# Optimization experiments

Hardware: AMD Instinct MI355X
Metric: run time of the kernel (lower is better)

The kernel has to match this reference:

```python
import jax, jax.numpy as jnp
import numpy as np
import math

B, S, D, H = 4, 2048, 1024, 16
HD = D // H

def setup_inputs() -> dict:
    key = jax.random.key(0)
    k = jax.random.split(key, 5)
    scale = 1.0 / math.sqrt(D)
    return {
        "x": jax.random.normal(k[0], (B, S, D), dtype=jnp.float32),
        "W_qkv": jax.random.normal(k[1], (D, 3 * D), dtype=jnp.float32) * scale,
        "b_qkv": jnp.zeros((3 * D,), dtype=jnp.float32),
        "W_out": jax.random.normal(k[2], (D, D), dtype=jnp.float32) * scale,
        "b_out": jnp.zeros((D,), dtype=jnp.float32),
    }

def reference(x, W_qkv, b_qkv, W_out, b_out):
    b, s, d = x.shape
    qkv = x @ W_qkv + b_qkv                       # [b, s, 3d]
    qkv = qkv.reshape(b, s, 3, H, HD)
    q, k, v = jnp.moveaxis(qkv, 2, 0)             # each [b, s, H, HD]
    q = jnp.transpose(q, (0, 2, 1, 3))            # [b, H, s, hd]
    k = jnp.transpose(k, (0, 2, 1, 3))
    v = jnp.transpose(v, (0, 2, 1, 3))
    scores = jnp.einsum('bhqd,bhkd->bhqk', q, k) / math.sqrt(HD)
    causal = jnp.tril(jnp.ones((s, s), dtype=bool))
    scores = jnp.where(causal, scores, -jnp.inf)
    weights = jax.nn.softmax(scores, axis=-1)     # dropout = identity (eval)
    attended = jnp.einsum('bhqk,bhkd->bhqd', weights, v)
    attended = jnp.transpose(attended, (0, 2, 1, 3)).reshape(b, s, d)
    return attended @ W_out + b_out
```

## Files before the change

### kernel.cpp

```cpp
#include <hip/hip_runtime.h>
#include <hip/hip_bf16.h>

typedef __attribute__((ext_vector_type(4))) float f32x4;
typedef __attribute__((ext_vector_type(16))) float f32x16;
typedef __attribute__((ext_vector_type(8))) short short8;

static constexpr int Ssz = 2048;
static constexpr int Dsz = 1024;

__device__ __forceinline__ unsigned short f2bf(float f){
  union { float f; unsigned u; } c; c.f = f;
  unsigned r = c.u + 0x7fffu + ((c.u >> 16) & 1u);
  return (unsigned short)(r >> 16);
}

__device__ __forceinline__ void gl2lds16(const void* g, void* l){
  __builtin_amdgcn_global_load_lds(
    (const __attribute__((address_space(1))) unsigned int*)g,
    (__attribute__((address_space(3))) unsigned int*)l, 16, 0, 0);
}

__device__ __forceinline__ unsigned cvtpk(float lo, float hi){
  unsigned r;
  asm("v_cvt_pk_bf16_f32 %0, %1, %2" : "=v"(r) : "v"(lo), "v"(hi));
  return r;
}

__device__ __forceinline__ void permswap(unsigned &a, unsigned &b){
  asm volatile("v_permlane32_swap_b32 %0, %1" : "+v"(a), "+v"(b));
}

__device__ __forceinline__ float xmax64(float x){
  float a = x, b;
  asm volatile("v_mov_b32 %0, %1" : "=v"(b) : "v"(a));
  asm volatile("v_permlane32_swap_b32 %0, %1" : "+v"(a), "+v"(b));
  return fmaxf(a, b);
}
__device__ __forceinline__ float xsum64(float x){
  float a = x, b;
  asm volatile("v_mov_b32 %0, %1" : "=v"(b) : "v"(a));
  asm volatile("v_permlane32_swap_b32 %0, %1" : "+v"(a), "+v"(b));
  return a + b;
}

__global__ void cvt_kernel(const float* __restrict__ in, unsigned short* __restrict__ out, int n){
  int i = (blockIdx.x * 256 + threadIdx.x) * 8;
  if (i >= n) return;
  float4 a = *(const float4*)(in + i);
  float4 b = *(const float4*)(in + i + 4);
  short8 o;
  o[0]=(short)f2bf(a.x); o[1]=(short)f2bf(a.y); o[2]=(short)f2bf(a.z); o[3]=(short)f2bf(a.w);
  o[4]=(short)f2bf(b.x); o[5]=(short)f2bf(b.y); o[6]=(short)f2bf(b.z); o[7]=(short)f2bf(b.w);
  *(short8*)(out + i) = o;
}

__global__ void transpose_kernel(const float* __restrict__ in, unsigned short* __restrict__ out,
                                 int R, int C){
  __shared__ float tile[32][33];
  int c0 = blockIdx.x * 32, r0 = blockIdx.y * 32;
  int tx = threadIdx.x, ty = threadIdx.y;
  #pragma unroll
  for (int k = 0; k < 4; ++k)
    tile[ty + 8*k][tx] = in[(size_t)(r0 + ty + 8*k) * C + c0 + tx];
  __syncthreads();
  #pragma unroll
  for (int k = 0; k < 4; ++k)
    out[(size_t)(c0 + ty + 8*k) * R + r0 + tx] = f2bf(tile[tx][ty + 8*k]);
}

__global__ __launch_bounds__(512, 2)
void gemm_qkv(const unsigned short* __restrict__ A, const unsigned short* __restrict__ Bt,
              const float* __restrict__ bias,
              unsigned short* __restrict__ Qp, unsigned short* __restrict__ Kp,
              unsigned short* __restrict__ Vtp)
{
  constexpr int K = 1024, NT = 16;
  __shared__ unsigned short ldsA[2][256 * 64];
  __shared__ unsigned short ldsB[2][256 * 64];
  const int tid = threadIdx.x;
  const int wid = tid >> 6, lane = tid & 63;
  const int lr = lane & 15, lg = lane >> 4;
  const int wm = wid >> 2, wn = wid & 3;

  int bid = blockIdx.x;
  int swz = (bid & 7) * 48 + (bid >> 3);
  const int m0 = (swz / 12) * 256, n0 = (swz % 12) * 256;

  const f32x4 vzero = {0.f, 0.f, 0.f, 0.f};
  f32x4 acc[8][4];
  #pragma unroll
  for (int i = 0; i < 8; ++i)
    #pragma unroll
    for (int j = 0; j < 4; ++j) acc[i][j] = vzero;

  auto stage = [&](int sigma){
    if (sigma >= 4 * NT) return;
    const int ts = sigma >> 2, ss = sigma & 3;
    const int buf = ts & 1;
    #pragma unroll
    for (int call = 0; call < 2; ++call){
      int c = call * 512 + tid;
      int rw = c >> 3, cc = c & 7;
      if (ss == 0 || ss == 3){
        int row = ((rw >> 5) << 6) + (rw & 31) + (ss == 3 ? 32 : 0);
        int sc = cc ^ (row & 7);
        gl2lds16(Bt + (size_t)(n0 + row) * K + ts * 64 + sc * 8,
                 &ldsB[buf][row * 64 + cc * 8]);
      } else {
        int row = ((rw >> 6) << 7) + (rw & 63) + (ss == 2 ? 64 : 0);
        int sc = cc ^ (row & 7);
        gl2lds16(A + (size_t)(m0 + row) * K + ts * 64 + sc * 8,
                 &ldsA[buf][row * 64 + cc * 8]);
      }
    }
  };

  short8 af[4][2], bf2[2][2];

  stage(0); stage(1); stage(2); stage(3); stage(4);
  asm volatile("s_waitcnt vmcnt(6)" ::: "memory");
  __builtin_amdgcn_sched_barrier(0);
  __builtin_amdgcn_s_barrier();

  #pragma unroll 1
  for (int t = 0; t < NT; ++t){
    const char* baA = (const char*)&ldsA[t & 1][0];
    const char* baB = (const char*)&ldsB[t & 1][0];

    #pragma unroll
    for (int ii = 0; ii < 4; ++ii)
      #pragma unroll
      for (int kk = 0; kk < 2; ++kk){
        int row = wm * 128 + ii * 16 + lr;
        int off = (row * 128 + lg * 16 + kk * 64) ^ ((row & 7) << 4);
        af[ii][kk] = *(const short8*)(baA + off);
      }
    #pragma unroll
    for (int jj = 0; jj < 2; ++jj)
      #pragma unroll
      for (int kk = 0; kk < 2; ++kk){
        int row = wn * 64 + jj * 16 + lr;
        int off = (row * 128 + lg * 16 + kk * 64) ^ ((row & 7) << 4);
        bf2[jj][kk] = *(const short8*)(baB + off);
      }
    stage(4 * t + 5);
    __builtin_amdgcn_s_barrier();
    asm volatile("s_waitcnt lgkmcnt(0)" ::: "memory");
    __builtin_amdgcn_sched_barrier(0);
    __builtin_amdgcn_s_setprio(1);
    #pragma unroll
    for (int ii = 0; ii < 4; ++ii)
      #pragma unroll
      for (int jj = 0; jj < 2; ++jj)
        #pragma unroll
        for (int kk = 0; kk < 2; ++kk)
          acc[ii][jj] = __builtin_amdgcn_mfma_f32_16x16x32_bf16(af[ii][kk], bf2[jj][kk], acc[ii][jj], 0, 0, 0);
    __builtin_amdgcn_s_setprio(0);
    asm volatile("s_waitcnt vmcnt(6)" ::: "memory");
    __builtin_amdgcn_sched_barrier(0);
    __builtin_amdgcn_s_barrier();

    #pragma unroll
    for (int ii = 0; ii < 4; ++ii)
      #pragma unroll
      for (int kk = 0; kk < 2; ++kk){
        int row = wm * 128 + 64 + ii * 16 + lr;
        int off = (row * 128 + lg * 16 + kk * 64) ^ ((row & 7) << 4);
        af[ii][kk] = *(const short8*)(baA + off);
      }
    stage(4 * t + 6);
    __builtin_amdgcn_s_barrier();
    asm volatile("s_waitcnt lgkmcnt(0)" ::: "memory");
    __builtin_amdgcn_sched_barrier(0);
    __builtin_amdgcn_s_setprio(1);
    #pragma unroll
    for (int ii = 0; ii < 4; ++ii)
      #pragma unroll
      for (int jj = 0; jj < 2; ++jj)
        #pragma unroll
        for (int kk = 0; kk < 2; ++kk)
          acc[4 + ii][jj] = __builtin_amdgcn_mfma_f32_16x16x32_bf16(af[ii][kk], bf2[jj][kk], acc[4 + ii][jj], 0, 0, 0);
    __builtin_amdgcn_s_setprio(0);
    asm volatile("s_waitcnt vmcnt(6)" ::: "memory");
    __builtin_amdgcn_sched_barrier(0);
    __builtin_amdgcn_s_barrier();

    #pragma unroll
    for (int jj = 0; jj < 2; ++jj)
      #pragma unroll
      for (int kk = 0; kk < 2; ++kk){
        int row = wn * 64 + 32 + jj * 16 + lr;
        int off = (row * 128 + lg * 16 + kk * 64) ^ ((row & 7) << 4);
        bf2[jj][kk] = *(const short8*)(baB + off);
      }
    stage(4 * t + 7);
    __builtin_amdgcn_s_barrier();
    asm volatile("s_waitcnt lgkmcnt(0)" ::: "memory");
    __builtin_amdgcn_sched_barrier(0);
    __builtin_amdgcn_s_setprio(1);
    #pragma unroll
    for (int ii = 0; ii < 4; ++ii)
      #pragma unroll
      for (int jj = 0; jj < 2; ++jj)
        #pragma unroll
        for (int kk = 0; kk < 2; ++kk)
          acc[4 + ii][2 + jj] = __builtin_amdgcn_mfma_f32_16x16x32_bf16(af[ii][kk], bf2[jj][kk], acc[4 + ii][2 + jj], 0, 0, 0);
    __builtin_amdgcn_s_setprio(0);
    __builtin_amdgcn_s_barrier();

    #pragma unroll
    for (int ii = 0; ii < 4; ++ii)
      #pragma unroll
      for (int kk = 0; kk < 2; ++kk){
        int row = wm * 128 + ii * 16 + lr;
        int off = (row * 128 + lg * 16 + kk * 64) ^ ((row & 7) << 4);
        af[ii][kk] = *(const short8*)(baA + off);
      }
    stage(4 * t + 8);
    __builtin_amdgcn_s_barrier();
    asm volatile("s_waitcnt lgkmcnt(0)" ::: "memory");
    __builtin_amdgcn_sched_barrier(0);
    __builtin_amdgcn_s_setprio(1);
    #pragma unroll
    for (int ii = 0; ii < 4; ++ii)
      #pragma unroll
      for (int jj = 0; jj < 2; ++jj)
        #pragma unroll
        for (int kk = 0; kk < 2; ++kk)
          acc[ii][2 + jj] = __builtin_amdgcn_mfma_f32_16x16x32_bf16(af[ii][kk], bf2[jj][kk], acc[ii][2 + jj], 0, 0, 0);
    __builtin_amdgcn_s_setprio(0);
    asm volatile("s_waitcnt vmcnt(6)" ::: "memory");
    __builtin_amdgcn_sched_barrier(0);
    __builtin_amdgcn_s_barrier();
  }

  asm volatile("s_waitcnt vmcnt(0)" ::: "memory");

  const float qscale = 0.125f * 1.4426950408889634f;
  #pragma unroll
  for (int i = 0; i < 8; ++i)
    #pragma unroll
    for (int j = 0; j < 4; ++j)
      #pragma unroll
      for (int r = 0; r < 4; ++r){
        int gm = m0 + wm * 128 + i * 16 + lg * 4 + r;
        int gn = n0 + wn * 64 + j * 16 + lr;
        float v = acc[i][j][r] + bias[gn];
        int which = gn >> 10;
        int h = (gn >> 6) & 15;
        int hd = gn & 63;
        int b = gm >> 11;
        int s = gm & 2047;
        size_t bh = (size_t)(b * 16 + h);
        if (which == 0)      Qp[(bh * Ssz + s) * 64 + hd] = f2bf(v * qscale);
        else if (which == 1) Kp[(bh * Ssz + s) * 64 + hd] = f2bf(v);
        else                 Vtp[(bh * 64 + hd) * Ssz + s] = f2bf(v);
      }
}

#define BM 128
#define BN 128
#define BKg 64

__global__ __launch_bounds__(256, 2)
void gemm_bt(const unsigned short* __restrict__ A, const unsigned short* __restrict__ Bt,
             int M, int N, int K,
             const float* __restrict__ bias, float* __restrict__ Out)
{
  __shared__ unsigned short ldsA[BM * BKg];
  __shared__ unsigned short ldsB[BN * BKg];
  const int tid = threadIdx.x;
  const int wid = tid >> 6;
  const int lane = tid & 63;
  const int lr = lane & 15, lg = lane >> 4;
  const int wr = wid >> 1, wc = wid & 1;
  const int m0 = blockIdx.y * BM, n0 = blockIdx.x * BN;

  const f32x4 vzero = {0.f, 0.f, 0.f, 0.f};
  f32x4 acc[4][4];
  #pragma unroll
  for (int i = 0; i < 4; ++i)
    #pragma unroll
    for (int j = 0; j < 4; ++j) acc[i][j] = vzero;

  for (int k0 = 0; k0 < K; k0 += BKg){
    __syncthreads();
    #pragma unroll
    for (int it = 0; it < 4; ++it){
      int c = it * 256 + tid;
      int row = c >> 3;
      int sc = (c & 7) ^ (row & 7);
      gl2lds16(A  + (size_t)(m0 + row) * K + k0 + sc * 8,
               (char*)ldsA + (it * 256 + wid * 64) * 16);
      gl2lds16(Bt + (size_t)(n0 + row) * K + k0 + sc * 8,
               (char*)ldsB + (it * 256 + wid * 64) * 16);
    }
    __syncthreads();
    #pragma unroll
    for (int kc = 0; kc < 2; ++kc){
      short8 af[4], bfr[4];
      #pragma unroll
      for (int i = 0; i < 4; ++i){
        int row = wr * 64 + i * 16 + lr;
        int off = row * 128 + lg * 16 + kc * 64;
        off ^= (row & 7) << 4;
        af[i] = *(const short8*)((const char*)ldsA + off);
      }
      #pragma unroll
      for (int j = 0; j < 4; ++j){
        int row = wc * 64 + j * 16 + lr;
        int off = row * 128 + lg * 16 + kc * 64;
        off ^= (row & 7) << 4;
        bfr[j] = *(const short8*)((const char*)ldsB + off);
      }
      #pragma unroll
      for (int i = 0; i < 4; ++i)
        #pragma unroll
        for (int j = 0; j < 4; ++j)
          acc[i][j] = __builtin_amdgcn_mfma_f32_16x16x32_bf16(af[i], bfr[j], acc[i][j], 0, 0, 0);
    }
  }

  #pragma unroll
  for (int i = 0; i < 4; ++i)
    #pragma unroll
    for (int j = 0; j < 4; ++j)
      #pragma unroll
      for (int r = 0; r < 4; ++r){
        int gm = m0 + wr * 64 + i * 16 + lg * 4 + r;
        int gn = n0 + wc * 64 + j * 16 + lr;
        Out[(size_t)gm * N + gn] = acc[i][j][r] + bias[gn];
      }
}

__global__ __launch_bounds__(256, 2)
void attn_kernel(const unsigned short* __restrict__ Qp, const unsigned short* __restrict__ Kp,
                 const unsigned short* __restrict__ Vtp, unsigned short* __restrict__ Att)
{
  __shared__ unsigned short ldsK[2][4096];
  __shared__ unsigned short ldsV[2][4096];
  const int tid = threadIdx.x;
  const int wid = tid >> 6;
  const int lane = tid & 63;
  const int lq = lane & 31;
  const int hi = lane >> 5;
  const int bh = blockIdx.y;
  const int b = bh >> 4, hh = bh & 15;

  #pragma unroll 1
  for (int job = 0; job < 2; ++job){
    const int qt = job ? (15 - (int)blockIdx.x) : (int)blockIdx.x;
    const int q0w = qt * 128 + wid * 32;
    const int qa = q0w + lq;
    const int nt = 2 * qt + 2;

    short8 qf[4];
    {
      const unsigned short* Qb = Qp + ((size_t)bh * Ssz + q0w + lq) * 64 + hi * 8;
      #pragma unroll
      for (int ks = 0; ks < 4; ++ks) qf[ks] = *(const short8*)(Qb + ks * 16);
    }

    f32x16 Ot[2];
    #pragma unroll
    for (int d = 0; d < 2; ++d)
      #pragma unroll
      for (int r = 0; r < 16; ++r) Ot[d][r] = 0.f;
    float mrun = -3e38f, lsum = 0.f;

    #pragma unroll
    for (int it = 0; it < 2; ++it){
      int c = it * 256 + tid;
      int row = c >> 3, sc = (c & 7) ^ (row & 7);
      gl2lds16(Kp  + ((size_t)bh * Ssz + row) * 64 + sc * 8,
               (char*)&ldsK[0][0] + (it * 256 + wid * 64) * 16);
      gl2lds16(Vtp + ((size_t)bh * 64 + row) * Ssz + sc * 8,
               (char*)&ldsV[0][0] + (it * 256 + wid * 64) * 16);
    }
    __syncthreads();

    for (int kt = 0; kt < nt; ++kt){
      const int cur = kt & 1;
      if (kt + 1 < nt){
        const int nxt = cur ^ 1;
        #pragma unroll
        for (int it = 0; it < 2; ++it){
          int c = it * 256 + tid;
          int row = c >> 3, sc = (c & 7) ^ (row & 7);
          gl2lds16(Kp  + ((size_t)bh * Ssz + (kt + 1) * 64 + row) * 64 + sc * 8,
                   (char*)&ldsK[nxt][0] + (it * 256 + wid * 64) * 16);
          gl2lds16(Vtp + ((size_t)bh * 64 + row) * Ssz + (kt + 1) * 64 + sc * 8,
                   (char*)&ldsV[nxt][0] + (it * 256 + wid * 64) * 16);
        }
      }

      if (kt * 64 <= q0w + 31){
        const char* Kb = (const char*)&ldsK[cur][0];
        const char* Vb = (const char*)&ldsV[cur][0];

        f32x16 S[2];
        #pragma unroll
        for (int kb = 0; kb < 2; ++kb)
          #pragma unroll
          for (int r = 0; r < 16; ++r) S[kb][r] = 0.f;
        #pragma unroll
        for (int ks = 0; ks < 4; ++ks){
          int col = 32 * ks + 16 * hi;
          int r0 = lq, r1 = 32 + lq;
          short8 k0 = *(const short8*)(Kb + ((r0 * 128 + col) ^ ((r0 & 7) << 4)));
          short8 k1 = *(const short8*)(Kb + ((r1 * 128 + col) ^ ((r1 & 7) << 4)));
          S[0] = __builtin_amdgcn_mfma_f32_32x32x16_bf16(k0, qf[ks], S[0], 0, 0, 0);
          S[1] = __builtin_amdgcn_mfma_f32_32x32x16_bf16(k1, qf[ks], S[1], 0, 0, 0);
        }

        if (kt * 64 + 63 > q0w){
          #pragma unroll
          for (int r = 0; r < 16; ++r){
            int keyb = kt * 64 + (r & 3) + ((r >> 2) << 3) + 4 * hi;
            if (keyb > qa)      S[0][r] = -3e38f;
            if (keyb + 32 > qa) S[1][r] = -3e38f;
          }
        }

        float t16[16];
        #pragma unroll
        for (int r = 0; r < 16; ++r) t16[r] = fmaxf(S[0][r], S[1][r]);
        float t8[8];
        #pragma unroll
        for (int r = 0; r < 8; ++r) t8[r] = fmaxf(t16[r], t16[r + 8]);
        float t4[4];
        #pragma unroll
        for (int r = 0; r < 4; ++r) t4[r] = fmaxf(t8[r], t8[r + 4]);
        float pmax = fmaxf(fmaxf(t4[0], t4[1]), fmaxf(t4[2], t4[3]));
        pmax = xmax64(pmax);

        if (!__all(pmax - mrun <= 8.0f)){
          float mn = fmaxf(mrun, pmax);
          float scl = __builtin_amdgcn_exp2f(mrun - mn);
          mrun = mn;
          lsum *= scl;
          #pragma unroll
          for (int d = 0; d < 2; ++d)
            #pragma unroll
            for (int r = 0; r < 16; ++r) Ot[d][r] *= scl;
        }

        #pragma unroll
        for (int kb = 0; kb < 2; ++kb)
          #pragma unroll
          for (int r = 0; r < 16; ++r)
            S[kb][r] = __builtin_amdgcn_exp2f(S[kb][r] - mrun);

        #pragma unroll
        for (int r = 0; r < 16; ++r) t16[r] = S[0][r] + S[1][r];
        #pragma unroll
        for (int r = 0; r < 8; ++r) t8[r] = t16[r] + t16[r + 8];
        #pragma unroll
        for (int r = 0; r < 4; ++r) t4[r] = t8[r] + t8[r + 4];
        float psum = (t4[0] + t4[1]) + (t4[2] + t4[3]);
        psum = xsum64(psum);
        lsum += psum;

        #pragma unroll
        for (int s = 0; s < 4; ++s){
          const int sb = s >> 1, s1 = s & 1;
          unsigned u0 = cvtpk(S[sb][8 * s1 + 0], S[sb][8 * s1 + 1]);
          unsigned u1 = cvtpk(S[sb][8 * s1 + 2], S[sb][8 * s1 + 3]);
          unsigned u2 = cvtpk(S[sb][8 * s1 + 4], S[sb][8 * s1 + 5]);
          unsigned u3 = cvtpk(S[sb][8 * s1 + 6], S[sb][8 * s1 + 7]);
          permswap(u0, u2);
          permswap(u1, u3);
          union { unsigned u[4]; short8 s8; } pb;
          pb.u[0] = u0; pb.u[1] = u1; pb.u[2] = u2; pb.u[3] = u3;

          int col = 32 * s + 16 * hi;
          int r0 = lq, r1 = 32 + lq;
          short8 v0 = *(const short8*)(Vb + ((r0 * 128 + col) ^ ((r0 & 7) << 4)));
          short8 v1 = *(const short8*)(Vb + ((r1 * 128 + col) ^ ((r1 & 7) << 4)));
          Ot[0] = __builtin_amdgcn_mfma_f32_32x32x16_bf16(v0, pb.s8, Ot[0], 0, 0, 0);
          Ot[1] = __builtin_amdgcn_mfma_f32_32x32x16_bf16(v1, pb.s8, Ot[1], 0, 0, 0);
        }
      }
      __syncthreads();
    }

    float inv = 1.0f / lsum;
    unsigned short* ep = &ldsK[0][0] + wid * 2048;
    #pragma unroll
    for (int d = 0; d < 2; ++d)
      #pragma unroll
      for (int g = 0; g < 4; ++g)
        #pragma unroll
        for (int cp = 0; cp < 2; ++cp){
          int r = g * 4 + cp * 2;
          unsigned w = cvtpk(Ot[d][r] * inv, Ot[d][r + 1] * inv);
          int dd = d * 32 + g * 8 + 4 * hi + cp * 2;
          int byte = lq * 128 + ((dd * 2) ^ ((lq & 7) << 4));
          *(unsigned*)((char*)ep + byte) = w;
        }
    __syncthreads();
    #pragma unroll
    for (int i = 0; i < 4; ++i){
      int qr = i * 8 + (lane >> 3);
      int cc = lane & 7;
      int byte = qr * 128 + ((cc * 16) ^ ((qr & 7) << 4));
      short8 vv = *(const short8*)((const char*)ep + byte);
      *(short8*)(Att + ((size_t)(b * Ssz + q0w + qr)) * Dsz + hh * 64 + cc * 8) = vv;
    }
    __syncthreads();
  }
}

extern "C" void kernel_launch(void* const* d_in, const int* in_sizes, int n_in,
                              void* d_out, int out_size, void* d_ws, size_t ws_size,
                              hipStream_t stream) {
  const float* x    = (const float*)d_in[0];
  const float* Wqkv = (const float*)d_in[1];
  const float* bqkv = (const float*)d_in[2];
  const float* Wout = (const float*)d_in[3];
  const float* bout = (const float*)d_in[4];
  float* out = (float*)d_out;

  unsigned short* xb    = (unsigned short*)d_ws;
  unsigned short* wqkvT = xb    + (size_t)8192 * 1024;
  unsigned short* woutT = wqkvT + (size_t)3072 * 1024;
  unsigned short* Qb    = woutT + (size_t)1024 * 1024;
  unsigned short* Kb    = Qb    + (size_t)8388608;
  unsigned short* Vtb   = Kb    + (size_t)8388608;
  unsigned short* Attb  = Vtb   + (size_t)8388608;

  cvt_kernel<<<4096, 256, 0, stream>>>(x, xb, 8388608);
  transpose_kernel<<<dim3(96, 32), dim3(32, 8), 0, stream>>>(Wqkv, wqkvT, 1024, 3072);
  transpose_kernel<<<dim3(32, 32), dim3(32, 8), 0, stream>>>(Wout, woutT, 1024, 1024);
  gemm_qkv<<<384, 512, 0, stream>>>(xb, wqkvT, bqkv, Qb, Kb, Vtb);
  attn_kernel<<<dim3(8, 64), 256, 0, stream>>>(Qb, Kb, Vtb, Attb);
  gemm_bt<<<dim3(8, 64), 256, 0, stream>>>(Attb, woutT, 8192, 1024, 1024, bout, out);
}
```

Measured before the change: 199.9 us.

## Keep low A fragments in registers to skip reload and deepen QKV GEMM prefetch

The QKV projection GEMM main loop now holds separate register sets for the low and high halves of the A tile. The fourth MFMA quarter reuses the low-half fragments instead of re-reading them from LDS. The global-to-LDS staging schedule is reworked so operands are issued further ahead, with seven stages in the prologue and loads for tile t+2 issued inside iteration t. Two of the vmcnt waits per iteration are dropped. This trades extra VGPRs (another 8 short8 fragments) for fewer LDS reads and fewer stalls, with some risk of register pressure or ordering hazards in the double-buffered LDS.

```diff
diff --git a/kernel.cpp b/kernel.cpp
--- a/kernel.cpp
+++ b/kernel.cpp
@@ -93,21 +93,20 @@
     #pragma unroll
     for (int j = 0; j < 4; ++j) acc[i][j] = vzero;
 
-  auto stage = [&](int sigma){
-    if (sigma >= 4 * NT) return;
-    const int ts = sigma >> 2, ss = sigma & 3;
+  auto stage = [&](int ts, int op){
+    if (ts >= NT) return;
     const int buf = ts & 1;
     #pragma unroll
     for (int call = 0; call < 2; ++call){
       int c = call * 512 + tid;
       int rw = c >> 3, cc = c & 7;
-      if (ss == 0 || ss == 3){
-        int row = ((rw >> 5) << 6) + (rw & 31) + (ss == 3 ? 32 : 0);
+      if (op == 0 || op == 3){
+        int row = ((rw >> 5) << 6) + (rw & 31) + (op == 3 ? 32 : 0);
         int sc = cc ^ (row & 7);
         gl2lds16(Bt + (size_t)(n0 + row) * K + ts * 64 + sc * 8,
                  &ldsB[buf][row * 64 + cc * 8]);
       } else {
-        int row = ((rw >> 6) << 7) + (rw & 63) + (ss == 2 ? 64 : 0);
+        int row = ((rw >> 6) << 7) + (rw & 63) + (op == 2 ? 64 : 0);
         int sc = cc ^ (row & 7);
         gl2lds16(A + (size_t)(m0 + row) * K + ts * 64 + sc * 8,
                  &ldsA[buf][row * 64 + cc * 8]);
@@ -115,9 +114,10 @@
     }
   };
 
-  short8 af[4][2], bf2[2][2];
-
-  stage(0); stage(1); stage(2); stage(3); stage(4);
+  short8 af_lo[4][2], af_hi[4][2], bfr[2][2];
+
+  stage(0, 0); stage(0, 1); stage(0, 2); stage(0, 3);
+  stage(1, 0); stage(1, 1); stage(1, 2);
   asm volatile("s_waitcnt vmcnt(6)" ::: "memory");
   __builtin_amdgcn_sched_barrier(0);
   __builtin_amdgcn_s_barrier();
@@ -133,7 +133,7 @@
       for (int kk = 0; kk < 2; ++kk){
         int row = wm * 128 + ii * 16 + lr;
         int off = (row * 128 + lg * 16 + kk * 64) ^ ((row & 7) << 4);
-        af[ii][kk] = *(const short8*)(baA + off);
+        af_lo[ii][kk] = *(const short8*)(baA + off);
       }
     #pragma unroll
     for (int jj = 0; jj < 2; ++jj)
@@ -141,9 +141,9 @@
       for (int kk = 0; kk < 2; ++kk){
         int row = wn * 64 + jj * 16 + lr;
         int off = (row * 128 + lg * 16 + kk * 64) ^ ((row & 7) << 4);
-        bf2[jj][kk] = *(const short8*)(baB + off);
-      }
-    stage(4 * t + 5);
+        bfr[jj][kk] = *(const short8*)(baB + off);
+      }
+    stage(t + 1, 3);
     __builtin_amdgcn_s_barrier();
     asm volatile("s_waitcnt lgkmcnt(0)" ::: "memory");
     __builtin_amdgcn_sched_barrier(0);
@@ -154,10 +154,8 @@
       for (int jj = 0; jj < 2; ++jj)
         #pragma unroll
         for (int kk = 0; kk < 2; ++kk)
-          acc[ii][jj] = __builtin_amdgcn_mfma_f32_16x16x32_bf16(af[ii][kk], bf2[jj][kk], acc[ii][jj], 0, 0, 0);
+          acc[ii][jj] = __builtin_amdgcn_mfma_f32_16x16x32_bf16(af_lo[ii][kk], bfr[jj][kk], acc[ii][jj], 0, 0, 0);
     __builtin_amdgcn_s_setprio(0);
-    asm volatile("s_waitcnt vmcnt(6)" ::: "memory");
-    __builtin_amdgcn_sched_barrier(0);
     __builtin_amdgcn_s_barrier();
 
     #pragma unroll
@@ -166,9 +164,9 @@
       for (int kk = 0; kk < 2; ++kk){
         int row = wm * 128 + 64 + ii * 16 + lr;
         int off = (row * 128 + lg * 16 + kk * 64) ^ ((row & 7) << 4);
-        af[ii][kk] = *(const short8*)(baA + off);
-      }
-    stage(4 * t + 6);
+        af_hi[ii][kk] = *(const short8*)(baA + off);
+      }
+    stage(t + 2, 0);
     __builtin_amdgcn_s_barrier();
     asm volatile("s_waitcnt lgkmcnt(0)" ::: "memory");
     __builtin_amdgcn_sched_barrier(0);
@@ -179,10 +177,8 @@
       for (int jj = 0; jj < 2; ++jj)
         #pragma unroll
         for (int kk = 0; kk < 2; ++kk)
-          acc[4 + ii][jj] = __builtin_amdgcn_mfma_f32_16x16x32_bf16(af[ii][kk], bf2[jj][kk], acc[4 + ii][jj], 0, 0, 0);
+          acc[4 + ii][jj] = __builtin_amdgcn_mfma_f32_16x16x32_bf16(af_hi[ii][kk], bfr[jj][kk], acc[4 + ii][jj], 0, 0, 0);
     __builtin_amdgcn_s_setprio(0);
-    asm volatile("s_waitcnt vmcnt(6)" ::: "memory");
-    __builtin_amdgcn_sched_barrier(0);
     __builtin_amdgcn_s_barrier();
 
     #pragma unroll
@@ -191,9 +187,9 @@
       for (int kk = 0; kk < 2; ++kk){
         int row = wn * 64 + 32 + jj * 16 + lr;
         int off = (row * 128 + lg * 16 + kk * 64) ^ ((row & 7) << 4);
-        bf2[jj][kk] = *(const short8*)(baB + off);
-      }
-    stage(4 * t + 7);
+        bfr[jj][kk] = *(const short8*)(baB + off);
+      }
+    stage(t + 2, 1);
     __builtin_amdgcn_s_barrier();
     asm volatile("s_waitcnt lgkmcnt(0)" ::: "memory");
     __builtin_amdgcn_sched_barrier(0);
@@ -204,30 +200,20 @@
       for (int jj = 0; jj < 2; ++jj)
         #pragma unroll
         for (int kk = 0; kk < 2; ++kk)
-          acc[4 + ii][2 + jj] = __builtin_amdgcn_mfma_f32_16x16x32_bf16(af[ii][kk], bf2[jj][kk], acc[4 + ii][2 + jj], 0, 0, 0);
+          acc[4 + ii][2 + jj] = __builtin_amdgcn_mfma_f32_16x16x32_bf16(af_hi[ii][kk], bfr[jj][kk], acc[4 + ii][2 + jj], 0, 0, 0);
     __builtin_amdgcn_s_setprio(0);
     __builtin_amdgcn_s_barrier();
 
+    stage(t + 2, 2);
+    __builtin_amdgcn_s_barrier();
+    __builtin_amdgcn_s_setprio(1);
     #pragma unroll
     for (int ii = 0; ii < 4; ++ii)
       #pragma unroll
-      for (int kk = 0; kk < 2; ++kk){
-        int row = wm * 128 + ii * 16 + lr;
-        int off = (row * 128 + lg * 16 + kk * 64) ^ ((row & 7) << 4);
-        af[ii][kk] = *(const short8*)(baA + off);
-      }
-    stage(4 * t + 8);
-    __builtin_amdgcn_s_barrier();
-    asm volatile("s_waitcnt lgkmcnt(0)" ::: "memory");
-    __builtin_amdgcn_sched_barrier(0);
-    __builtin_amdgcn_s_setprio(1);
-    #pragma unroll
-    for (int ii = 0; ii < 4; ++ii)
-      #pragma unroll
       for (int jj = 0; jj < 2; ++jj)
         #pragma unroll
         for (int kk = 0; kk < 2; ++kk)
-          acc[ii][2 + jj] = __builtin_amdgcn_mfma_f32_16x16x32_bf16(af[ii][kk], bf2[jj][kk], acc[ii][2 + jj], 0, 0, 0);
+          acc[ii][2 + jj] = __builtin_amdgcn_mfma_f32_16x16x32_bf16(af_lo[ii][kk], bfr[jj][kk], acc[ii][2 + jj], 0, 0, 0);
     __builtin_amdgcn_s_setprio(0);
     asm volatile("s_waitcnt vmcnt(6)" ::: "memory");
     __builtin_amdgcn_sched_barrier(0);
```

Result: slower. 210.7 us (+5.4%).
